# Kernel tuning notes

Hardware: AMD Instinct MI355X
Metric: run time of the kernel (lower is better)

The kernel has to match this reference:

```python
import jax, jax.numpy as jnp
import numpy as np

N = 50000      # nodes
E = 800000     # edges (avg degree 16)
IN, EMB, HID, OUT = 128, 256, 256, 128
KS = (25000, 12500)  # absolute top-k node counts per pooling level
NEG = -1e9


def setup_inputs() -> dict:
    key = jax.random.key(0)
    k = jax.random.split(key, 20)
    s = 0.05
    rn = lambda kk, shp: (jax.random.normal(kk, shp, jnp.float32) * s)
    return {
        "features": jax.random.normal(k[0], (N, IN), jnp.float32),
        "src": jax.random.randint(k[1], (E,), 0, N, dtype=jnp.int32),
        "dst": jax.random.randint(k[2], (E,), 0, N, dtype=jnp.int32),
        "W_embed": rn(k[3], (IN, EMB)), "b_embed": jnp.zeros((EMB,), jnp.float32),
        "W_enc0": rn(k[4], (EMB, HID)), "b_enc0": jnp.zeros((HID,), jnp.float32),
        "W_enc1": rn(k[5], (HID, HID)), "b_enc1": jnp.zeros((HID,), jnp.float32),
        "W_p0": rn(k[6], (HID, 1)), "b_p0": jnp.zeros((1,), jnp.float32),
        "W_p1": rn(k[7], (HID, 1)), "b_p1": jnp.zeros((1,), jnp.float32),
        "W_bot": rn(k[8], (HID, HID)), "b_bot": jnp.zeros((HID,), jnp.float32),
        "W_dec0": rn(k[9], (HID, HID)), "b_dec0": jnp.zeros((HID,), jnp.float32),
        "W_dec1": rn(k[10], (HID, OUT)), "b_dec1": jnp.zeros((OUT,), jnp.float32),
    }


def _gcn(h, src, dst, emask, W, b, act):
    """DGL GraphConv, norm='both': D_out^{-1/2} A D_in^{-1/2} h W + b, deg clamped >=1.
    emask: float [E] validity mask for edges of the current (sub)graph."""
    n = h.shape[0]
    deg_out = jnp.clip(jax.ops.segment_sum(emask, src, num_segments=n), 1.0)
    deg_in = jnp.clip(jax.ops.segment_sum(emask, dst, num_segments=n), 1.0)
    msg = (h * (deg_out ** -0.5)[:, None])[src] * emask[:, None]  # [E, F]
    agg = jax.ops.segment_sum(msg, dst, num_segments=n)
    out = (agg * (deg_in ** -0.5)[:, None]) @ W + b
    return jax.nn.relu(out) if act else out


def _forward(features, src, dst, W_embed, b_embed, W_enc0, b_enc0, W_enc1, b_enc1,
             W_p0, b_p0, W_p1, b_p1, W_bot, b_bot, W_dec0, b_dec0, W_dec1, b_dec1):
    n = features.shape[0]
    ones_e = jnp.ones((src.shape[0],), features.dtype)
    enc = [(W_enc0, b_enc0), (W_enc1, b_enc1)]
    pools = [(W_p0, b_p0), (W_p1, b_p1)]
    dec = [(W_dec0, b_dec0), (W_dec1, b_dec1)]
    L = len(KS)

    h = _gcn(features, src, dst, ones_e, W_embed, b_embed, True)
    masks = [jnp.ones((n,), features.dtype)]  # node mask per graph level
    hidden = []
    for i in range(L):  # encoder (dropout = eval-mode identity)
        m = masks[i]
        em = m[src] * m[dst]
        h = _gcn(h, src, dst, em, enc[i][0], enc[i][1], True) * m[:, None]
        hidden.append(h)
        # gPool: sigmoid projection score, top-k node selection, gate by score
        scores = jax.nn.sigmoid(h @ pools[i][0] + pools[i][1])[:, 0]
        _, idx = jax.lax.top_k(jnp.where(m > 0, scores, NEG), KS[i])
        nm = jnp.zeros((n,), features.dtype).at[idx].set(1.0)
        h = h * (scores * nm)[:, None]
        masks.append(nm)
    mL = masks[L]
    emL = mL[src] * mL[dst]
    h = _gcn(h, src, dst, emL, W_bot, b_bot, True) * mL[:, None]
    for i in range(L):  # decoder: gUnpool (identity under full-rep masking) + skip + GCN
        j = L - 1 - i
        h = h + hidden[j]
        m = masks[j]
        em = m[src] * m[dst]
        act = i < L - 1  # last decoder layer has no activation
        h = _gcn(h, src, dst, em, dec[i][0], dec[i][1], act) * m[:, None]
    return h


def reference(features, src, dst, W_embed, b_embed, W_enc0, b_enc0, W_enc1, b_enc1,
              W_p0, b_p0, W_p1, b_p1, W_bot, b_bot, W_dec0, b_dec0, W_dec1, b_dec1):
    return _forward(features, src, dst, W_embed, b_embed, W_enc0, b_enc0, W_enc1, b_enc1,
                    W_p0, b_p0, W_p1, b_p1, W_bot, b_bot, W_dec0, b_dec0, W_dec1, b_dec1)
```

## Files before the change

### kernel.cpp

```cpp
#include <hip/hip_runtime.h>
#include <hip/hip_bf16.h>
#include <type_traits>

__global__ void hist_kernel(const int* __restrict__ src, const int* __restrict__ dst,
                            int* __restrict__ deg_out, int* __restrict__ deg_in, int E) {
    int e = blockIdx.x * blockDim.x + threadIdx.x;
    if (e < E) {
        atomicAdd(&deg_out[src[e]], 1);
        atomicAdd(&deg_in[dst[e]], 1);
    }
}

__global__ void scan_kernel(const int* __restrict__ deg, int* __restrict__ row_ptr,
                            int* __restrict__ cursor, int n) {
    __shared__ int wsum[16];
    __shared__ int running;
    int tid = threadIdx.x, lane = tid & 63, wid = tid >> 6;
    if (tid == 0) running = 0;
    __syncthreads();
    for (int base = 0; base < n; base += 1024) {
        int i = base + tid;
        int v = (i < n) ? deg[i] : 0;
        int incl = v;
        #pragma unroll
// ... 158 lines not shown
    float tv = t[node];
    if (MASKED && tv == 0.f) return;
    int e0 = row_ptr[node], e1 = row_ptr[node + 1];
    const float4* X4 = (const float4*)X;
    float ax = 0.f, ay = 0.f, az = 0.f, aw = 0.f;
    int e = e0;
    for (; e + 3 < e1; e += 4) {
        int u0 = col[e], u1 = col[e + 1], u2 = col[e + 2], u3 = col[e + 3];
        float s0 = s[u0], s1 = s[u1], s2 = s[u2], s3 = s[u3];
        if (!MASKED) {
            float4 x0 = X4[(size_t)u0 * 64 + f4];
            float4 x1 = X4[(size_t)u1 * 64 + f4];
            float4 x2 = X4[(size_t)u2 * 64 + f4];
            float4 x3 = X4[(size_t)u3 * 64 + f4];
            ax += s0 * x0.x; ay += s0 * x0.y; az += s0 * x0.z; aw += s0 * x0.w;
            ax += s1 * x1.x; ay += s1 * x1.y; az += s1 * x1.z; aw += s1 * x1.w;
            ax += s2 * x2.x; ay += s2 * x2.y; az += s2 * x2.z; aw += s2 * x2.w;
            ax += s3 * x3.x; ay += s3 * x3.y; az += s3 * x3.z; aw += s3 * x3.w;
        } else {
            if (s0 != 0.f) { float4 x = X4[(size_t)u0 * 64 + f4];
                ax += s0 * x.x; ay += s0 * x.y; az += s0 * x.z; aw += s0 * x.w; }
            if (s1 != 0.f) { float4 x = X4[(size_t)u1 * 64 + f4];
                ax += s1 * x.x; ay += s1 * x.y; az += s1 * x.z; aw += s1 * x.w; }
            if (s2 != 0.f) { float4 x = X4[(size_t)u2 * 64 + f4];
                ax += s2 * x.x; ay += s2 * x.y; az += s2 * x.z; aw += s2 * x.w; }
            if (s3 != 0.f) { float4 x = X4[(size_t)u3 * 64 + f4];
                ax += s3 * x.x; ay += s3 * x.y; az += s3 * x.z; aw += s3 * x.w; }
        }
    }
    for (; e < e1; ++e) {
        int u = col[e];
        float sc = s[u];
        if (!MASKED || sc != 0.f) {
            float4 xv = X4[(size_t)u * 64 + f4];
            ax += sc * xv.x; ay += sc * xv.y; az += sc * xv.z; aw += sc * xv.w;
        }
    }
    if (SPLIT) {
        ushort4 hv, lv;
        split4(ax * tv, ay * tv, az * tv, aw * tv, hv, lv);
        *(ushort4*)&oh[(size_t)node * 256 + f4 * 4] = hv;
        *(ushort4*)&ol[(size_t)node * 256 + f4 * 4] = lv;
    } else {
        float4 r; r.x = ax * tv; r.y = ay * tv; r.z = az * tv; r.w = aw * tv;
        ((float4*)out)[(size_t)node * 64 + f4] = r;
    }
}

__global__ void agg_bias_128_kernel(const int* __restrict__ row_ptr, const int* __restrict__ col,
                                    const float* __restrict__ P, const float* __restrict__ t,
                                    const float* __restrict__ bias, float* __restrict__ out, int n) {
    int tid = threadIdx.x;
    int node = blockIdx.x * 8 + (tid >> 5);
    int f4 = tid & 31;
    if (node >= n) return;
    int e0 = row_ptr[node], e1 = row_ptr[node + 1];
    const float4* P4 = (const float4*)P;
    float ax = 0.f, ay = 0.f, az = 0.f, aw = 0.f;
    int e = e0;
    for (; e + 3 < e1; e += 4) {
        int u0 = col[e], u1 = col[e + 1], u2 = col[e + 2], u3 = col[e + 3];
        float4 x0 = P4[(size_t)u0 * 32 + f4];
        float4 x1 = P4[(size_t)u1 * 32 + f4];
        float4 x2 = P4[(size_t)u2 * 32 + f4];
        float4 x3 = P4[(size_t)u3 * 32 + f4];
        ax += x0.x; ay += x0.y; az += x0.z; aw += x0.w;
        ax += x1.x; ay += x1.y; az += x1.z; aw += x1.w;
        ax += x2.x; ay += x2.y; az += x2.z; aw += x2.w;
        ax += x3.x; ay += x3.y; az += x3.z; aw += x3.w;
    }
    for (; e < e1; ++e) {
        int u = col[e];
        float4 q = P4[(size_t)u * 32 + f4];
        ax += q.x; ay += q.y; az += q.z; aw += q.w;
    }
    float tv = t[node];
    float4 bv = ((const float4*)bias)[f4];
    float4 r;
    r.x = ax * tv + bv.x; r.y = ay * tv + bv.y;
    r.z = az * tv + bv.z; r.w = aw * tv + bv.w;
    ((float4*)out)[(size_t)node * 32 + f4] = r;
}

__global__ void add_split_kernel(const float* __restrict__ A, const float* __restrict__ B,
                                 const float* __restrict__ mask, const float* __restrict__ rs,
                                 unsigned short* __restrict__ oh, unsigned short* __restrict__ ol,
                                 int n4) {
    int i = blockIdx.x * blockDim.x + threadIdx.x;
    if (i >= n4) return;
    int row = i >> 6;
    float4 a = ((const float4*)A)[i];
    float4 b = ((const float4*)B)[i];
    if (mask[row] == 0.f) { a.x = 0.f; a.y = 0.f; a.z = 0.f; a.w = 0.f; }
    float r = rs[row];
    ushort4 hv, lv;
    split4((a.x + b.x) * r, (a.y + b.y) * r, (a.z + b.z) * r, (a.w + b.w) * r, hv, lv);
    size_t o = (size_t)row * 256 + (size_t)(i & 63) * 4;
    *(ushort4*)&oh[o] = hv;
    *(ushort4*)&ol[o] = lv;
}


__global__ void wsplit_all_kernel(const float* __restrict__ W0, const float* __restrict__ W1,
                                  const float* __restrict__ W2, const float* __restrict__ W3,
                                  const float* __restrict__ W4, const float* __restrict__ W5,
                                  unsigned short* __restrict__ H, unsigned short* __restrict__ L) {
    int i = blockIdx.x * blockDim.x + threadIdx.x;
    const float* W; int rel, base, outIdx;
    if (i < 32768) { W = W0; rel = i; base = 0;
        int k = rel >> 8, nn = rel & 255; outIdx = nn * 128 + k; }
    else if (i < 98304) { W = W1; rel = i - 32768; base = 32768;
        int k = rel >> 8, nn = rel & 255; outIdx = nn * 256 + k; }
    else if (i < 163840) { W = W2; rel = i - 98304; base = 98304;
        int k = rel >> 8, nn = rel & 255; outIdx = nn * 256 + k; }
    else if (i < 229376) { W = W3; rel = i - 163840; base = 163840;
        int k = rel >> 8, nn = rel & 255; outIdx = nn * 256 + k; }
    else if (i < 294912) { W = W4; rel = i - 229376; base = 229376;
        int k = rel >> 8, nn = rel & 255; outIdx = nn * 256 + k; }
    else { W = W5; rel = i - 294912; base = 294912;
        int k = rel >> 7, nn = rel & 127; outIdx = nn * 256 + k; }
    float x = W[rel];
    unsigned short h = f2bf(x);
    H[base + outIdx] = h;
    L[base + outIdx] = f2bf(x - bf2f(h));
}

template <bool RELU>
__global__ __launch_bounds__(256) void gemm_mfma_kernel(
    const unsigned short* __restrict__ Ah, const unsigned short* __restrict__ Al,
    const unsigned short* __restrict__ Wh, const unsigned short* __restrict__ Wl,
    const float* __restrict__ bias, float* __restrict__ C, int M, int K, int Nn) {
    __shared__ __align__(16) short sAh[64][40];
    __shared__ __align__(16) short sAl[64][40];
    __shared__ __align__(16) short sWh[128][40];
    __shared__ __align__(16) short sWl[128][40];
    int tid = threadIdx.x;
    int bm = blockIdx.x * 64, bn = blockIdx.y * 128;
    int lane = tid & 63, wid = tid >> 6;
    int lr = lane & 15, kg = lane >> 4;
    int arow = tid >> 2, akq = (tid & 3) * 8;
    int wn = tid >> 1, wkh = (tid & 1) * 16;
    const unsigned short* ahp = Ah + (size_t)(bm + arow) * K + akq;
    const unsigned short* alp = Al + (size_t)(bm + arow) * K + akq;
    const unsigned short* whp = Wh + (size_t)(bn + wn) * K + wkh;
    const unsigned short* wlp = Wl + (size_t)(bn + wn) * K + wkh;
    f32x4 acc[4][2];
    #pragma unroll
    for (int i = 0; i < 4; ++i)
        #pragma unroll
        for (int j = 0; j < 2; ++j) acc[i][j] = (f32x4){0.f, 0.f, 0.f, 0.f};
    for (int k0 = 0; k0 < K; k0 += 32) {
        short8v aH = *(const short8v*)(ahp + k0);
        short8v aL = *(const short8v*)(alp + k0);
        short8v w0 = *(const short8v*)(whp + k0);
        short8v w1 = *(const short8v*)(whp + k0 + 8);
        short8v w2 = *(const short8v*)(wlp + k0);
        short8v w3 = *(const short8v*)(wlp + k0 + 8);
        __syncthreads();
        *(short8v*)&sAh[arow][akq] = aH;
        *(short8v*)&sAl[arow][akq] = aL;
        *(short8v*)&sWh[wn][wkh] = w0;
        *(short8v*)&sWh[wn][wkh + 8] = w1;
        *(short8v*)&sWl[wn][wkh] = w2;
        *(short8v*)&sWl[wn][wkh + 8] = w3;
        __syncthreads();
        short8v ah[4], al[4], bh[2], bl[2];
        #pragma unroll
        for (int mf = 0; mf < 4; ++mf) {
            ah[mf] = *(const short8v*)&sAh[mf * 16 + lr][kg * 8];
            al[mf] = *(const short8v*)&sAl[mf * 16 + lr][kg * 8];
        }
        #pragma unroll
        for (int nf = 0; nf < 2; ++nf) {
            int c = wid * 32 + nf * 16 + lr;
            bh[nf] = *(const short8v*)&sWh[c][kg * 8];
            bl[nf] = *(const short8v*)&sWl[c][kg * 8];
        }
        #pragma unroll
        for (int mf = 0; mf < 4; ++mf)
            #pragma unroll
            for (int nf = 0; nf < 2; ++nf) {
                acc[mf][nf] = __builtin_amdgcn_mfma_f32_16x16x32_bf16(ah[mf], bh[nf], acc[mf][nf], 0, 0, 0);
                acc[mf][nf] = __builtin_amdgcn_mfma_f32_16x16x32_bf16(ah[mf], bl[nf], acc[mf][nf], 0, 0, 0);
                acc[mf][nf] = __builtin_amdgcn_mfma_f32_16x16x32_bf16(al[mf], bh[nf], acc[mf][nf], 0, 0, 0);
            }
    }
    #pragma unroll
    for (int mf = 0; mf < 4; ++mf) {
        #pragma unroll
        for (int nf = 0; nf < 2; ++nf) {
            int col = bn + wid * 32 + nf * 16 + lr;
            float bv = bias ? bias[col] : 0.f;
            #pragma unroll
            for (int r = 0; r < 4; ++r) {
                int grow = bm + mf * 16 + kg * 4 + r;
                if (grow < M) {
                    float x = acc[mf][nf][r] + bv;
                    if (RELU) x = fmaxf(x, 0.f);
                    C[(size_t)grow * Nn + col] = x;
                }
            }
        }
    }
}

template <bool RELU>
__global__ __launch_bounds__(256) void gemm_rows_mfma_kernel(
    const unsigned short* __restrict__ Ah, const unsigned short* __restrict__ Al,
    const unsigned short* __restrict__ Wh, const unsigned short* __restrict__ Wl,
    const float* __restrict__ bias, const int* __restrict__ idx, int Mc,
    float* __restrict__ C, int K, int Nn) {
    __shared__ __align__(16) short sAh[64][40];
    __shared__ __align__(16) short sAl[64][40];
    __shared__ __align__(16) short sWh[128][40];
    __shared__ __align__(16) short sWl[128][40];
    __shared__ int ridx[64];
    int tid = threadIdx.x;
    int bm = blockIdx.x * 64, bn = blockIdx.y * 128;
    int lane = tid & 63, wid = tid >> 6;
    int lr = lane & 15, kg = lane >> 4;
    int arow = tid >> 2, akq = (tid & 3) * 8;
    int wn = tid >> 1, wkh = (tid & 1) * 16;
    if (tid < 64) {
        int r = bm + tid;
        ridx[tid] = (r < Mc) ? idx[r] : idx[0];
    }
    __syncthreads();
    int rA = ridx[arow];
    const unsigned short* ahp = Ah + (size_t)rA * K + akq;
    const unsigned short* alp = Al + (size_t)rA * K + akq;
    const unsigned short* whp = Wh + (size_t)(bn + wn) * K + wkh;
    const unsigned short* wlp = Wl + (size_t)(bn + wn) * K + wkh;
    f32x4 acc[4][2];
    #pragma unroll
    for (int i = 0; i < 4; ++i)
        #pragma unroll
        for (int j = 0; j < 2; ++j) acc[i][j] = (f32x4){0.f, 0.f, 0.f, 0.f};
    for (int k0 = 0; k0 < K; k0 += 32) {
        short8v aH = *(const short8v*)(ahp + k0);
        short8v aL = *(const short8v*)(alp + k0);
        short8v w0 = *(const short8v*)(whp + k0);
        short8v w1 = *(const short8v*)(whp + k0 + 8);
        short8v w2 = *(const short8v*)(wlp + k0);
        short8v w3 = *(const short8v*)(wlp + k0 + 8);
        __syncthreads();
        *(short8v*)&sAh[arow][akq] = aH;
        *(short8v*)&sAl[arow][akq] = aL;
        *(short8v*)&sWh[wn][wkh] = w0;
        *(short8v*)&sWh[wn][wkh + 8] = w1;
        *(short8v*)&sWl[wn][wkh] = w2;
        *(short8v*)&sWl[wn][wkh + 8] = w3;
        __syncthreads();
        short8v ah[4], al[4], bh[2], bl[2];
        #pragma unroll
        for (int mf = 0; mf < 4; ++mf) {
            ah[mf] = *(const short8v*)&sAh[mf * 16 + lr][kg * 8];
            al[mf] = *(const short8v*)&sAl[mf * 16 + lr][kg * 8];
        }
        #pragma unroll
        for (int nf = 0; nf < 2; ++nf) {
            int c = wid * 32 + nf * 16 + lr;
            bh[nf] = *(const short8v*)&sWh[c][kg * 8];
            bl[nf] = *(const short8v*)&sWl[c][kg * 8];
        }
        #pragma unroll
        for (int mf = 0; mf < 4; ++mf)
            #pragma unroll
            for (int nf = 0; nf < 2; ++nf) {
                acc[mf][nf] = __builtin_amdgcn_mfma_f32_16x16x32_bf16(ah[mf], bh[nf], acc[mf][nf], 0, 0, 0);
                acc[mf][nf] = __builtin_amdgcn_mfma_f32_16x16x32_bf16(ah[mf], bl[nf], acc[mf][nf], 0, 0, 0);
                acc[mf][nf] = __builtin_amdgcn_mfma_f32_16x16x32_bf16(al[mf], bh[nf], acc[mf][nf], 0, 0, 0);
            }
    }
    #pragma unroll
    for (int mf = 0; mf < 4; ++mf) {
        #pragma unroll
        for (int nf = 0; nf < 2; ++nf) {
            int col = bn + wid * 32 + nf * 16 + lr;
            float bv = bias[col];
            #pragma unroll
            for (int r = 0; r < 4; ++r) {
                int lrow = mf * 16 + kg * 4 + r;
                if (bm + lrow < Mc) {
                    int grow = ridx[lrow];
                    float x = acc[mf][nf][r] + bv;
                    if (RELU) x = fmaxf(x, 0.f);
                    C[(size_t)grow * Nn + col] = x;
                }
            }
        }
    }
}

template <bool RELU>
__global__ __launch_bounds__(256) void gemm_kernel(const float* __restrict__ A,
                                                   const float* __restrict__ W,
                                                   const float* __restrict__ bias,
                                                   const float* __restrict__ mask,
                                                   const float* __restrict__ rowscale,
                                                   float* __restrict__ C, int M, int K, int Nn) {
    __shared__ float As[16][68];
    __shared__ float Bs[16][132];
    int tid = threadIdx.x;
    int bm = blockIdx.x * 64, bn = blockIdx.y * 128;
    int mA = tid >> 2, kqA = (tid & 3) * 4;
    int kB = tid >> 4, nqB = (tid & 15) * 8;
    int tm = (tid >> 4) * 4, tn = (tid & 15) * 4;
    float acc[4][8] = {};
    float rs = rowscale ? rowscale[bm + mA] : 1.f;
    for (int k0 = 0; k0 < K; k0 += 16) {
        float4 av = *(const float4*)(A + (size_t)(bm + mA) * K + k0 + kqA);
        As[kqA + 0][mA] = av.x * rs; As[kqA + 1][mA] = av.y * rs;
        As[kqA + 2][mA] = av.z * rs; As[kqA + 3][mA] = av.w * rs;
        const float* wp = W + (size_t)(k0 + kB) * Nn + bn + nqB;
        *(float4*)&Bs[kB][nqB]     = *(const float4*)wp;
        *(float4*)&Bs[kB][nqB + 4] = *(const float4*)(wp + 4);
        __syncthreads();
        #pragma unroll
        for (int kk = 0; kk < 16; ++kk) {
            float4 a  = *(const float4*)&As[kk][tm];
            float4 b0 = *(const float4*)&Bs[kk][tn];
            float4 b1 = *(const float4*)&Bs[kk][tn + 64];
            float ar[4] = {a.x, a.y, a.z, a.w};
            float br[8] = {b0.x, b0.y, b0.z, b0.w, b1.x, b1.y, b1.z, b1.w};
            #pragma unroll
            for (int i2 = 0; i2 < 4; i2++)
                #pragma unroll
                for (int j = 0; j < 8; j++) acc[i2][j] += ar[i2] * br[j];
        }
        __syncthreads();
    }
    #pragma unroll
    for (int i2 = 0; i2 < 4; i2++) {
        int row = bm + tm + i2;
        if (row < M) {
            float mv = mask ? mask[row] : 1.f;
            float o[8];
            #pragma unroll
            for (int j = 0; j < 8; j++) {
                int cj = (j < 4) ? (tn + j) : (64 + tn + j - 4);
                float x = acc[i2][j] + (bias ? bias[bn + cj] : 0.f);
                if (RELU) x = fmaxf(x, 0.f);
                o[j] = x * mv;
            }
            float* cp = C + (size_t)row * Nn + bn;
            *(float4*)(cp + tn)      = make_float4(o[0], o[1], o[2], o[3]);
            *(float4*)(cp + 64 + tn) = make_float4(o[4], o[5], o[6], o[7]);
        }
    }
}

__global__ void score_kernel(const float* __restrict__ H, const float* __restrict__ Wp,
                             const float* __restrict__ bp, const float* __restrict__ mask,
                             float* __restrict__ scores, float* __restrict__ keys, int n) {
    int lane = threadIdx.x & 63;
    int node = blockIdx.x * 4 + (threadIdx.x >> 6);
    if (node >= n) return;
    float4 hv = ((const float4*)(H + (size_t)node * 256))[lane];
    float4 wq = ((const float4*)Wp)[lane];
    float d = hv.x * wq.x + hv.y * wq.y + hv.z * wq.z + hv.w * wq.w;
    #pragma unroll
    for (int off = 32; off > 0; off >>= 1) d += __shfl_down(d, off);
    if (lane == 0) {
        float sc = 1.f / (1.f + expf(-(d + bp[0])));
        scores[node] = sc;
        keys[node] = (mask && mask[node] == 0.f) ? -1e9f : sc;
    }
}

__device__ __forceinline__ unsigned key_u(float f) {
    unsigned u = __float_as_uint(f);
// ... 127 lines not shown
    if (tid == 0) *tie_cnt = 0;
    int K = sel[1];
    int base = tid * 64;
    int local = 0;
    #pragma unroll 8
    for (int b = 0; b < 64; ++b) local += hist[base + b];
    arr[tid] = local;
    __syncthreads();
    for (int off = 1; off < 1024; off <<= 1) {
        int v = (tid + off < 1024) ? arr[tid + off] : 0;
        __syncthreads();
        arr[tid] += v;
        __syncthreads();
    }
    int above = arr[tid] - local;
    if (above < K && arr[tid] >= K) {
        int run = above;
        for (int b = base + 63; b >= base; --b) {
            int c = hist[b];
            if (run + c >= K) {
                sel[2] = (int)((((unsigned)sel[0]) << 16) | (unsigned)b);
                sel[3] = K - run;
                break;
            }
            run += c;
        }
    }
}

__global__ void topk_mark(const float* __restrict__ keys, const float* __restrict__ scores,
                          const int* __restrict__ sel, float* __restrict__ nm,
                          float* __restrict__ gate, int* __restrict__ tie_list,
                          int* __restrict__ tie_cnt, int n) {
    int i = blockIdx.x * blockDim.x + threadIdx.x;
    if (i >= n) return;
    unsigned Tkey = (unsigned)sel[2];
    unsigned u = key_u(keys[i]);
    float v = 0.f;
    if (u > Tkey) v = 1.f;
    else if (u == Tkey) { int p = atomicAdd(tie_cnt, 1); tie_list[p] = i; }
    nm[i] = v;
    gate[i] = v * scores[i];
}

__global__ void topk_ties(const float* __restrict__ scores, const int* __restrict__ sel,
                          const int* __restrict__ tie_list, const int* __restrict__ tie_cnt,
                          float* __restrict__ nm, float* __restrict__ gate) {
    int cnt = *tie_cnt;
    int need = sel[3];
    for (int j = threadIdx.x; j < cnt; j += blockDim.x) {
        int idx = tie_list[j];
        int rank = 0;
        for (int k2 = 0; k2 < cnt; ++k2) rank += (tie_list[k2] < idx) ? 1 : 0;
        if (rank < need) { nm[idx] = 1.f; gate[idx] = scores[idx]; }
    }
}

__global__ void compact_kernel(const float* __restrict__ nm, int* __restrict__ idx,
                               int* __restrict__ cnt, int n) {
    int i = blockIdx.x * blockDim.x + threadIdx.x;
    if (i < n && nm[i] != 0.f) {
        int p = atomicAdd(cnt, 1);
        idx[p] = i;
    }
}

__global__ void add_mask_kernel(float* __restrict__ A, const float* __restrict__ B,
                                const float* __restrict__ mask, int n4) {
    int i = blockIdx.x * blockDim.x + threadIdx.x;
    if (i < n4) {
        float4 a = ((float4*)A)[i];
        float4 b = ((const float4*)B)[i];
        if (mask && mask[i >> 6] == 0.f) { a.x = 0.f; a.y = 0.f; a.z = 0.f; a.w = 0.f; }
        a.x += b.x; a.y += b.y; a.z += b.z; a.w += b.w;
        ((float4*)A)[i] = a;
    }
}

extern "C" void kernel_launch(void* const* d_in, const int* in_sizes, int n_in,
                              void* d_out, int out_size, void* d_ws, size_t ws_size,
                              hipStream_t stream) {
    const int n = in_sizes[0] / 128;
    const int E = in_sizes[1];
    const int NPAD = ((n + 63) / 64) * 64;
    const int K1 = 25000, K2 = 12500;

    const float* features = (const float*)d_in[0];
    const int* src = (const int*)d_in[1];
    const int* dst = (const int*)d_in[2];
    const float* W_embed = (const float*)d_in[3];
    const float* b_embed = (const float*)d_in[4];
    const float* W_enc0  = (const float*)d_in[5];
    const float* b_enc0  = (const float*)d_in[6];
    const float* W_enc1  = (const float*)d_in[7];
    const float* b_enc1  = (const float*)d_in[8];
    const float* W_p0    = (const float*)d_in[9];
    const float* b_p0    = (const float*)d_in[10];
    const float* W_p1    = (const float*)d_in[11];
    const float* b_p1    = (const float*)d_in[12];
    const float* W_bot   = (const float*)d_in[13];
    const float* b_bot   = (const float*)d_in[14];
    const float* W_dec0  = (const float*)d_in[15];
    const float* b_dec0  = (const float*)d_in[16];
    const float* W_dec1  = (const float*)d_in[17];
    const float* b_dec1  = (const float*)d_in[18];
    float* out_f = (float*)d_out;

    char* ws = (char*)d_ws;
    size_t off = 0;
    auto alloc = [&](size_t bytes) -> void* {
        void* p = ws + off;
        off += (bytes + 255) & ~(size_t)255;
        return p;
    };
    (void)alloc(256);
    int* row_ptr  = (int*)alloc((size_t)(n + 1) * 4);
    int* cursor   = (int*)alloc((size_t)n * 4);
    int* col      = (int*)alloc((size_t)E * 4);
    int* deg_out_i= (int*)alloc((size_t)n * 4);
    int* deg_in_i = (int*)alloc((size_t)n * 4);
    float* so_m1  = (float*)alloc((size_t)n * 4);
    float* si_m1  = (float*)alloc((size_t)n * 4);
    float* so_m2  = (float*)alloc((size_t)n * 4);
    float* si_m2  = (float*)alloc((size_t)n * 4);
    float* sarr   = (float*)alloc((size_t)n * 4);
    float* tarr   = (float*)alloc((size_t)n * 4);
    float* scores1= (float*)alloc((size_t)n * 4);
    float* keys1  = (float*)alloc((size_t)n * 4);
    float* scores2= (float*)alloc((size_t)n * 4);
    float* keys2  = (float*)alloc((size_t)n * 4);
    float* nm1    = (float*)alloc((size_t)n * 4);
    float* gate1  = (float*)alloc((size_t)n * 4);
    float* nm2    = (float*)alloc((size_t)n * 4);
    float* gate2  = (float*)alloc((size_t)n * 4);
    size_t big = (size_t)NPAD * 256 * 4;
    float* A = (float*)alloc(big);
    float* B = (float*)alloc(big);
    float* C = (float*)alloc(big);
    float* D = (float*)alloc(big);
    unsigned short* Dh = (unsigned short*)D;
    unsigned short* Dl = Dh + (size_t)NPAD * 256;
    unsigned short* Dh128 = Dh;
    unsigned short* Dl128 = Dh + (size_t)NPAD * 128;
    int* rhist    = (int*)alloc(65536 * 4);
    int* sel      = (int*)alloc(256);
    int* tie_cnt  = (int*)alloc(256);
    int* tie_list = (int*)alloc((size_t)n * 4);
    float* s0     = (float*)alloc((size_t)n * 4);
    float* t0     = (float*)alloc((size_t)n * 4);
    int* idx1     = (int*)alloc((size_t)n * 4);
    int* idx2     = (int*)alloc((size_t)n * 4);
    int* ccnt     = (int*)alloc(256);
    const int WO_EMBED = 0, WO_ENC0 = 32768, WO_ENC1 = 98304,
              WO_BOT = 163840, WO_DEC0 = 229376, WO_DEC1 = 294912;
    const int WTOT = 327680;
    unsigned short* wsph = (unsigned short*)alloc((size_t)WTOT * 2);
    unsigned short* wspl = (unsigned short*)alloc((size_t)WTOT * 2);
    bool fast = (off <= ws_size);

    dim3 blk(256);
    int gE = (E + 255) / 256;
    int gN = (n + 255) / 256;
    int gAgg256 = (n + 3) / 4;
    int gAgg128 = (n + 7) / 8;
    int gScore = (n + 3) / 4;
    dim3 gemm_g(NPAD / 64, 2);
    dim3 gemm_g128(NPAD / 64, 1);
    dim3 gemm_gK1((K1 + 63) / 64, 2);
    dim3 gemm_gK2((K2 + 63) / 64, 2);
    int gAdd = (n * 64 + 255) / 256;

    auto run_topk = [&](const float* keys, const float* scores, float* nm, float* gate, int K) {
        if (fast) {
            hipMemsetAsync(rhist, 0, 65536 * 4, stream);
            topk_hist1<<<gN, blk, 0, stream>>>(keys, n, rhist);
            topk_scan1<<<1, 1024, 0, stream>>>(rhist, K, sel);
            hipMemsetAsync(rhist, 0, 65536 * 4, stream);
            topk_hist2<<<gN, blk, 0, stream>>>(keys, n, sel, rhist);
            topk_scan2<<<1, 1024, 0, stream>>>(rhist, sel, tie_cnt);
            topk_mark<<<gN, blk, 0, stream>>>(keys, scores, sel, nm, gate, tie_list, tie_cnt, n);
            topk_ties<<<1, 256, 0, stream>>>(scores, sel, tie_list, tie_cnt, nm, gate);
        } else {
            topk_kernel<<<1, 1024, 0, stream>>>(keys, scores, nm, gate, n, K);
        }
    };
    float* sF = fast ? s0 : sarr;
    float* tF = fast ? t0 : tarr;

    if (fast) {
        wsplit_all_kernel<<<WTOT / 256, blk, 0, stream>>>(W_embed, W_enc0, W_enc1, W_bot,
                                                          W_dec0, W_dec1, wsph, wspl);
    }

    hipMemsetAsync(deg_out_i, 0, (size_t)n * 4, stream);
    hipMemsetAsync(deg_in_i, 0, (size_t)n * 4, stream);
    hist_kernel<<<gE, blk, 0, stream>>>(src, dst, deg_out_i, deg_in_i, E);
    scan_kernel<<<1, 1024, 0, stream>>>(deg_in_i, row_ptr, cursor, n);
    fill_kernel<<<gE, blk, 0, stream>>>(src, dst, cursor, col, E);
    sort_rows_kernel<<<gN, blk, 0, stream>>>(row_ptr, col, n);

    scale_full_kernel<<<gN, blk, 0, stream>>>(deg_out_i, deg_in_i, sF, tF, n);

    if (fast) {
        agg_feat_128_kernel<true><<<gAgg128, blk, 0, stream>>>(row_ptr, col, features, sF, tF,
                                                               nullptr, Dh128, Dl128, n);
        gemm_mfma_kernel<true><<<gemm_g, blk, 0, stream>>>(Dh128, Dl128, wsph + WO_EMBED,
                                                           wspl + WO_EMBED, b_embed, A, n, 128, 256);
    } else {
        agg_feat_128_kernel<false><<<gAgg128, blk, 0, stream>>>(row_ptr, col, features, sF, tF,
                                                                D, nullptr, nullptr, n);
        gemm_kernel<true><<<gemm_g, blk, 0, stream>>>(D, W_embed, b_embed, nullptr, nullptr, A, n, 128, 256);
    }

    if (fast) {
        agg_f32_256_kernel<false, true><<<gAgg256, blk, 0, stream>>>(row_ptr, col, A, sF, tF,
                                                                     nullptr, Dh, Dl, n);
        gemm_mfma_kernel<true><<<gemm_g, blk, 0, stream>>>(Dh, Dl, wsph + WO_ENC0, wspl + WO_ENC0,
                                                           b_enc0, B, n, 256, 256);
    } else {
        agg_f32_256_kernel<false, false><<<gAgg256, blk, 0, stream>>>(row_ptr, col, A, sF, tF,
                                                                      D, nullptr, nullptr, n);
        gemm_kernel<true><<<gemm_g, blk, 0, stream>>>(D, W_enc0, b_enc0, nullptr, nullptr, B, n, 256, 256);
    }

    score_kernel<<<gScore, blk, 0, stream>>>(B, W_p0, b_p0, nullptr, scores1, keys1, n);
    run_topk(keys1, scores1, nm1, gate1, K1);
    if (fast) {
        hipMemsetAsync(ccnt, 0, 4, stream);
        compact_kernel<<<gN, blk, 0, stream>>>(nm1, idx1, ccnt, n);
    }

    hipMemsetAsync(so_m1, 0, (size_t)n * 4, stream);
    out_deg_mask_kernel<<<gE, blk, 0, stream>>>(src, dst, nm1, so_m1, E);
    in_deg_mask_kernel<<<gN, blk, 0, stream>>>(row_ptr, col, nm1, si_m1, n);
    scale_mask_kernel<<<gN, blk, 0, stream>>>(gate1, nm1, so_m1, si_m1, sarr, tarr, n);
    if (fast) {
        agg_f32_256_kernel<true, true><<<gAgg256, blk, 0, stream>>>(row_ptr, col, B, sarr, tarr,
                                                                    nullptr, Dh, Dl, n);
        gemm_rows_mfma_kernel<true><<<gemm_gK1, blk, 0, stream>>>(Dh, Dl, wsph + WO_ENC1,
                                                                  wspl + WO_ENC1, b_enc1, idx1, K1, C, 256, 256);
    } else {
        agg_f32_256_kernel<true, false><<<gAgg256, blk, 0, stream>>>(row_ptr, col, B, sarr, tarr,
                                                                     D, nullptr, nullptr, n);
        gemm_kernel<true><<<gemm_g, blk, 0, stream>>>(D, W_enc1, b_enc1, nm1, nullptr, C, n, 256, 256);
    }

    score_kernel<<<gScore, blk, 0, stream>>>(C, W_p1, b_p1, nm1, scores2, keys2, n);
    run_topk(keys2, scores2, nm2, gate2, K2);
    if (fast) {
        hipMemsetAsync(ccnt + 1, 0, 4, stream);
        compact_kernel<<<gN, blk, 0, stream>>>(nm2, idx2, ccnt + 1, n);
    }

    hipMemsetAsync(so_m2, 0, (size_t)n * 4, stream);
    out_deg_mask_kernel<<<gE, blk, 0, stream>>>(src, dst, nm2, so_m2, E);
    in_deg_mask_kernel<<<gN, blk, 0, stream>>>(row_ptr, col, nm2, si_m2, n);
    scale_mask_kernel<<<gN, blk, 0, stream>>>(gate2, nm2, so_m2, si_m2, sarr, tarr, n);
    if (fast) {
        agg_f32_256_kernel<true, true><<<gAgg256, blk, 0, stream>>>(row_ptr, col, C, sarr, tarr,
                                                                    nullptr, Dh, Dl, n);
        gemm_rows_mfma_kernel<true><<<gemm_gK2, blk, 0, stream>>>(Dh, Dl, wsph + WO_BOT,
                                                                  wspl + WO_BOT, b_bot, idx2, K2, A, 256, 256);
    } else {
        agg_f32_256_kernel<true, false><<<gAgg256, blk, 0, stream>>>(row_ptr, col, C, sarr, tarr,
                                                                     D, nullptr, nullptr, n);
        gemm_kernel<true><<<gemm_g, blk, 0, stream>>>(D, W_bot, b_bot, nm2, nullptr, A, n, 256, 256);
    }

    add_mask_kernel<<<gAdd, blk, 0, stream>>>(A, C, fast ? nm2 : nullptr, n * 64);
    scale_mask_kernel<<<gN, blk, 0, stream>>>(nm1, nm1, so_m1, si_m1, sarr, tarr, n);
    if (fast) {
        agg_f32_256_kernel<true, true><<<gAgg256, blk, 0, stream>>>(row_ptr, col, A, sarr, tarr,
                                                                    nullptr, Dh, Dl, n);
        gemm_rows_mfma_kernel<true><<<gemm_gK1, blk, 0, stream>>>(Dh, Dl, wsph + WO_DEC0,
                                                                  wspl + WO_DEC0, b_dec0, idx1, K1, A, 256, 256);
    } else {
        agg_f32_256_kernel<true, false><<<gAgg256, blk, 0, stream>>>(row_ptr, col, A, sarr, tarr,
                                                                     D, nullptr, nullptr, n);
        gemm_kernel<true><<<gemm_g, blk, 0, stream>>>(D, W_dec0, b_dec0, nm1, nullptr, A, n, 256, 256);
    }

    if (fast) {
        add_split_kernel<<<gAdd, blk, 0, stream>>>(A, B, nm1, sF, Dh, Dl, n * 64);
        gemm_mfma_kernel<false><<<gemm_g128, blk, 0, stream>>>(Dh, Dl, wsph + WO_DEC1,
                                                               wspl + WO_DEC1, nullptr, C, n, 256, 128);
    } else {
        add_mask_kernel<<<gAdd, blk, 0, stream>>>(A, B, nullptr, n * 64);
        scale_full_kernel<<<gN, blk, 0, stream>>>(deg_out_i, deg_in_i, sarr, tarr, n);
        gemm_kernel<false><<<gemm_g128, blk, 0, stream>>>(A, W_dec1, nullptr, nullptr, sF, C, n, 256, 128);
    }
    agg_bias_128_kernel<<<gAgg128, blk, 0, stream>>>(row_ptr, col, C, tF, b_dec1, out_f, n);

    (void)n_in; (void)out_size;
}
```

Before: 1.146 ms.

## Enlarge MFMA GEMM tiles to 128x128 and fuse add-split into dec1 GEMM

The split-bf16 MFMA GEMM kernels move from a 64x128 tile to a 128x128 tile, with each wave computing a 64x64 sub-tile. This gives more reuse per LDS load and halves the number of row blocks. The last decoder layer's add, mask, scale and bf16 hi/lo split is fused into the GEMM A-tile load, so the intermediate Dh/Dl buffers are no longer written and re-read. The two degree memsets are merged into one. The cost is more LDS and registers per block, which may lower occupancy, and the padded row count changes, so grids for the fallback path use separate dimensions.

Result: no change. 1.143 ms (-0.3%).

```diff
diff --git a/kernel.cpp b/kernel.cpp
--- a/kernel.cpp
+++ b/kernel.cpp
@@ -264,24 +264,6 @@
     ((float4*)out)[(size_t)node * 32 + f4] = r;
 }
 
-__global__ void add_split_kernel(const float* __restrict__ A, const float* __restrict__ B,
-                                 const float* __restrict__ mask, const float* __restrict__ rs,
-                                 unsigned short* __restrict__ oh, unsigned short* __restrict__ ol,
-                                 int n4) {
-    int i = blockIdx.x * blockDim.x + threadIdx.x;
-    if (i >= n4) return;
-    int row = i >> 6;
-    float4 a = ((const float4*)A)[i];
-    float4 b = ((const float4*)B)[i];
-    if (mask[row] == 0.f) { a.x = 0.f; a.y = 0.f; a.z = 0.f; a.w = 0.f; }
-    float r = rs[row];
-    ushort4 hv, lv;
-    split4((a.x + b.x) * r, (a.y + b.y) * r, (a.z + b.z) * r, (a.w + b.w) * r, hv, lv);
-    size_t o = (size_t)row * 256 + (size_t)(i & 63) * 4;
-    *(ushort4*)&oh[o] = hv;
-    *(ushort4*)&ol[o] = lv;
-}
-
 
 __global__ void wsplit_all_kernel(const float* __restrict__ W0, const float* __restrict__ W1,
                                   const float* __restrict__ W2, const float* __restrict__ W3,
@@ -308,74 +290,71 @@
 }
 
 template <bool RELU>
-__global__ __launch_bounds__(256) void gemm_mfma_kernel(
+__global__ __launch_bounds__(256, 3) void gemm_mfma_kernel(
     const unsigned short* __restrict__ Ah, const unsigned short* __restrict__ Al,
     const unsigned short* __restrict__ Wh, const unsigned short* __restrict__ Wl,
     const float* __restrict__ bias, float* __restrict__ C, int M, int K, int Nn) {
-    __shared__ __align__(16) short sAh[64][40];
-    __shared__ __align__(16) short sAl[64][40];
+    __shared__ __align__(16) short sAh[128][40];
+    __shared__ __align__(16) short sAl[128][40];
     __shared__ __align__(16) short sWh[128][40];
     __shared__ __align__(16) short sWl[128][40];
     int tid = threadIdx.x;
-    int bm = blockIdx.x * 64, bn = blockIdx.y * 128;
+    int bm = blockIdx.x * 128, bn = blockIdx.y * 128;
     int lane = tid & 63, wid = tid >> 6;
+    int wr = (wid >> 1) * 64, wc = (wid & 1) * 64;
     int lr = lane & 15, kg = lane >> 4;
-    int arow = tid >> 2, akq = (tid & 3) * 8;
-    int wn = tid >> 1, wkh = (tid & 1) * 16;
+    int arow = tid >> 1, akq = (tid & 1) * 16;
     const unsigned short* ahp = Ah + (size_t)(bm + arow) * K + akq;
     const unsigned short* alp = Al + (size_t)(bm + arow) * K + akq;
-    const unsigned short* whp = Wh + (size_t)(bn + wn) * K + wkh;
-    const unsigned short* wlp = Wl + (size_t)(bn + wn) * K + wkh;
-    f32x4 acc[4][2];
+    const unsigned short* whp = Wh + (size_t)(bn + arow) * K + akq;
+    const unsigned short* wlp = Wl + (size_t)(bn + arow) * K + akq;
+    f32x4 acc[4][4];
     #pragma unroll
     for (int i = 0; i < 4; ++i)
         #pragma unroll
-        for (int j = 0; j < 2; ++j) acc[i][j] = (f32x4){0.f, 0.f, 0.f, 0.f};
+        for (int j = 0; j < 4; ++j) acc[i][j] = (f32x4){0.f, 0.f, 0.f, 0.f};
     for (int k0 = 0; k0 < K; k0 += 32) {
-        short8v aH = *(const short8v*)(ahp + k0);
-        short8v aL = *(const short8v*)(alp + k0);
+        short8v a0 = *(const short8v*)(ahp + k0);
+        short8v a1 = *(const short8v*)(ahp + k0 + 8);
+        short8v l0 = *(const short8v*)(alp + k0);
+        short8v l1 = *(const short8v*)(alp + k0 + 8);
         short8v w0 = *(const short8v*)(whp + k0);
         short8v w1 = *(const short8v*)(whp + k0 + 8);
-        short8v w2 = *(const short8v*)(wlp + k0);
-        short8v w3 = *(const short8v*)(wlp + k0 + 8);
-        __syncthreads();
-        *(short8v*)&sAh[arow][akq] = aH;
-        *(short8v*)&sAl[arow][akq] = aL;
-        *(short8v*)&sWh[wn][wkh] = w0;
-        *(short8v*)&sWh[wn][wkh + 8] = w1;
-        *(short8v*)&sWl[wn][wkh] = w2;
-        *(short8v*)&sWl[wn][wkh + 8] = w3;
-        __syncthreads();
-        short8v ah[4], al[4], bh[2], bl[2];
+        short8v v0 = *(const short8v*)(wlp + k0);
+        short8v v1 = *(const short8v*)(wlp + k0 + 8);
+        __syncthreads();
+        *(short8v*)&sAh[arow][akq] = a0; *(short8v*)&sAh[arow][akq + 8] = a1;
+        *(short8v*)&sAl[arow][akq] = l0; *(short8v*)&sAl[arow][akq + 8] = l1;
+        *(short8v*)&sWh[arow][akq] = w0; *(short8v*)&sWh[arow][akq + 8] = w1;
+        *(short8v*)&sWl[arow][akq] = v0; *(short8v*)&sWl[arow][akq + 8] = v1;
+        __syncthreads();
+        short8v ah[4], al[4];
         #pragma unroll
         for (int mf = 0; mf < 4; ++mf) {
-            ah[mf] = *(const short8v*)&sAh[mf * 16 + lr][kg * 8];
-            al[mf] = *(const short8v*)&sAl[mf * 16 + lr][kg * 8];
-        }
-        #pragma unroll
-        for (int nf = 0; nf < 2; ++nf) {
-            int c = wid * 32 + nf * 16 + lr;
-            bh[nf] = *(const short8v*)&sWh[c][kg * 8];
-            bl[nf] = *(const short8v*)&sWl[c][kg * 8];
-        }
-        #pragma unroll
-        for (int mf = 0; mf < 4; ++mf)
+            ah[mf] = *(const short8v*)&sAh[wr + mf * 16 + lr][kg * 8];
+            al[mf] = *(const short8v*)&sAl[wr + mf * 16 + lr][kg * 8];
+        }
+        #pragma unroll
+        for (int nf = 0; nf < 4; ++nf) {
+            short8v bh = *(const short8v*)&sWh[wc + nf * 16 + lr][kg * 8];
+            short8v bl = *(const short8v*)&sWl[wc + nf * 16 + lr][kg * 8];
             #pragma unroll
-            for (int nf = 0; nf < 2; ++nf) {
-                acc[mf][nf] = __builtin_amdgcn_mfma_f32_16x16x32_bf16(ah[mf], bh[nf], acc[mf][nf], 0, 0, 0);
-                acc[mf][nf] = __builtin_amdgcn_mfma_f32_16x16x32_bf16(ah[mf], bl[nf], acc[mf][nf], 0, 0, 0);
-                acc[mf][nf] = __builtin_amdgcn_mfma_f32_16x16x32_bf16(al[mf], bh[nf], acc[mf][nf], 0, 0, 0);
+            for (int mf = 0; mf < 4; ++mf) {
+                acc[mf][nf] = __builtin_amdgcn_mfma_f32_16x16x32_bf16(ah[mf], bh, acc[mf][nf], 0, 0, 0);
+                acc[mf][nf] = __builtin_amdgcn_mfma_f32_16x16x32_bf16(ah[mf], bl, acc[mf][nf], 0, 0, 0);
+                acc[mf][nf] = __builtin_amdgcn_mfma_f32_16x16x32_bf16(al[mf], bh, acc[mf][nf], 0, 0, 0);
             }
+        }
     }
     #pragma unroll
     for (int mf = 0; mf < 4; ++mf) {
         #pragma unroll
-        for (int nf = 0; nf < 2; ++nf) {
-            int col = bn + wid * 32 + nf * 16 + lr;
+        for (int nf = 0; nf < 4; ++nf) {
+            int col = bn + wc + nf * 16 + lr;
             float bv = bias ? bias[col] : 0.f;
             #pragma unroll
             for (int r = 0; r < 4; ++r) {
-                int grow = bm + mf * 16 + kg * 4 + r;
+                int grow = bm + wr + mf * 16 + kg * 4 + r;
                 if (grow < M) {
                     float x = acc[mf][nf][r] + bv;
                     if (RELU) x = fmaxf(x, 0.f);
@@ -387,23 +366,23 @@
 }
 
 template <bool RELU>
-__global__ __launch_bounds__(256) void gemm_rows_mfma_kernel(
+__global__ __launch_bounds__(256, 3) void gemm_rows_mfma_kernel(
     const unsigned short* __restrict__ Ah, const unsigned short* __restrict__ Al,
     const unsigned short* __restrict__ Wh, const unsigned short* __restrict__ Wl,
     const float* __restrict__ bias, const int* __restrict__ idx, int Mc,
     float* __restrict__ C, int K, int Nn) {
-    __shared__ __align__(16) short sAh[64][40];
-    __shared__ __align__(16) short sAl[64][40];
+    __shared__ __align__(16) short sAh[128][40];
+    __shared__ __align__(16) short sAl[128][40];
     __shared__ __align__(16) short sWh[128][40];
     __shared__ __align__(16) short sWl[128][40];
-    __shared__ int ridx[64];
+    __shared__ int ridx[128];
     int tid = threadIdx.x;
-    int bm = blockIdx.x * 64, bn = blockIdx.y * 128;
+    int bm = blockIdx.x * 128, bn = blockIdx.y * 128;
     int lane = tid & 63, wid = tid >> 6;
+    int wr = (wid >> 1) * 64, wc = (wid & 1) * 64;
     int lr = lane & 15, kg = lane >> 4;
-    int arow = tid >> 2, akq = (tid & 3) * 8;
-    int wn = tid >> 1, wkh = (tid & 1) * 16;
-    if (tid < 64) {
+    int arow = tid >> 1, akq = (tid & 1) * 16;
+    if (tid < 128) {
         int r = bm + tid;
         ridx[tid] = (r < Mc) ? idx[r] : idx[0];
     }
@@ -411,64 +390,146 @@
     int rA = ridx[arow];
     const unsigned short* ahp = Ah + (size_t)rA * K + akq;
     const unsigned short* alp = Al + (size_t)rA * K + akq;
-    const unsigned short* whp = Wh + (size_t)(bn + wn) * K + wkh;
-    const unsigned short* wlp = Wl + (size_t)(bn + wn) * K + wkh;
-    f32x4 acc[4][2];
+    const unsigned short* whp = Wh + (size_t)(bn + arow) * K + akq;
+    const unsigned short* wlp = Wl + (size_t)(bn + arow) * K + akq;
+    f32x4 acc[4][4];
     #pragma unroll
     for (int i = 0; i < 4; ++i)
         #pragma unroll
-        for (int j = 0; j < 2; ++j) acc[i][j] = (f32x4){0.f, 0.f, 0.f, 0.f};
+        for (int j = 0; j < 4; ++j) acc[i][j] = (f32x4){0.f, 0.f, 0.f, 0.f};
     for (int k0 = 0; k0 < K; k0 += 32) {
-        short8v aH = *(const short8v*)(ahp + k0);
-        short8v aL = *(const short8v*)(alp + k0);
+        short8v a0 = *(const short8v*)(ahp + k0);
+        short8v a1 = *(const short8v*)(ahp + k0 + 8);
+        short8v l0 = *(const short8v*)(alp + k0);
+        short8v l1 = *(const short8v*)(alp + k0 + 8);
         short8v w0 = *(const short8v*)(whp + k0);
         short8v w1 = *(const short8v*)(whp + k0 + 8);
-        short8v w2 = *(const short8v*)(wlp + k0);
-        short8v w3 = *(const short8v*)(wlp + k0 + 8);
-        __syncthreads();
-        *(short8v*)&sAh[arow][akq] = aH;
-        *(short8v*)&sAl[arow][akq] = aL;
-        *(short8v*)&sWh[wn][wkh] = w0;
-        *(short8v*)&sWh[wn][wkh + 8] = w1;
-        *(short8v*)&sWl[wn][wkh] = w2;
-        *(short8v*)&sWl[wn][wkh + 8] = w3;
-        __syncthreads();
-        short8v ah[4], al[4], bh[2], bl[2];
+        short8v v0 = *(const short8v*)(wlp + k0);
+        short8v v1 = *(const short8v*)(wlp + k0 + 8);
+        __syncthreads();
+        *(short8v*)&sAh[arow][akq] = a0; *(short8v*)&sAh[arow][akq + 8] = a1;
+        *(short8v*)&sAl[arow][akq] = l0; *(short8v*)&sAl[arow][akq + 8] = l1;
+        *(short8v*)&sWh[arow][akq] = w0; *(short8v*)&sWh[arow][akq + 8] = w1;
+        *(short8v*)&sWl[arow][akq] = v0; *(short8v*)&sWl[arow][akq + 8] = v1;
+        __syncthreads();
+        short8v ah[4], al[4];
         #pragma unroll
         for (int mf = 0; mf < 4; ++mf) {
-            ah[mf] = *(const short8v*)&sAh[mf * 16 + lr][kg * 8];
-            al[mf] = *(const short8v*)&sAl[mf * 16 + lr][kg * 8];
-        }
-        #pragma unroll
-        for (int nf = 0; nf < 2; ++nf) {
-            int c = wid * 32 + nf * 16 + lr;
-            bh[nf] = *(const short8v*)&sWh[c][kg * 8];
-            bl[nf] = *(const short8v*)&sWl[c][kg * 8];
-        }
-        #pragma unroll
-        for (int mf = 0; mf < 4; ++mf)
+            ah[mf] = *(const short8v*)&sAh[wr + mf * 16 + lr][kg * 8];
+            al[mf] = *(const short8v*)&sAl[wr + mf * 16 + lr][kg * 8];
+        }
+        #pragma unroll
+        for (int nf = 0; nf < 4; ++nf) {
+            short8v bh = *(const short8v*)&sWh[wc + nf * 16 + lr][kg * 8];
+            short8v bl = *(const short8v*)&sWl[wc + nf * 16 + lr][kg * 8];
             #pragma unroll
-            for (int nf = 0; nf < 2; ++nf) {
-                acc[mf][nf] = __builtin_amdgcn_mfma_f32_16x16x32_bf16(ah[mf], bh[nf], acc[mf][nf], 0, 0, 0);
-                acc[mf][nf] = __builtin_amdgcn_mfma_f32_16x16x32_bf16(ah[mf], bl[nf], acc[mf][nf], 0, 0, 0);
-                acc[mf][nf] = __builtin_amdgcn_mfma_f32_16x16x32_bf16(al[mf], bh[nf], acc[mf][nf], 0, 0, 0);
+            for (int mf = 0; mf < 4; ++mf) {
+                acc[mf][nf] = __builtin_amdgcn_mfma_f32_16x16x32_bf16(ah[mf], bh, acc[mf][nf], 0, 0, 0);
+                acc[mf][nf] = __builtin_amdgcn_mfma_f32_16x16x32_bf16(ah[mf], bl, acc[mf][nf], 0, 0, 0);
+                acc[mf][nf] = __builtin_amdgcn_mfma_f32_16x16x32_bf16(al[mf], bh, acc[mf][nf], 0, 0, 0);
             }
+        }
     }
     #pragma unroll
     for (int mf = 0; mf < 4; ++mf) {
         #pragma unroll
-        for (int nf = 0; nf < 2; ++nf) {
-            int col = bn + wid * 32 + nf * 16 + lr;
+        for (int nf = 0; nf < 4; ++nf) {
+            int col = bn + wc + nf * 16 + lr;
             float bv = bias[col];
             #pragma unroll
             for (int r = 0; r < 4; ++r) {
-                int lrow = mf * 16 + kg * 4 + r;
+                int lrow = wr + mf * 16 + kg * 4 + r;
                 if (bm + lrow < Mc) {
                     int grow = ridx[lrow];
                     float x = acc[mf][nf][r] + bv;
                     if (RELU) x = fmaxf(x, 0.f);
                     C[(size_t)grow * Nn + col] = x;
                 }
+            }
+        }
+    }
+}
+
+__global__ __launch_bounds__(256, 3) void gemm_dec1_kernel(
+    const float* __restrict__ A, const float* __restrict__ B,
+    const float* __restrict__ mask, const float* __restrict__ rs,
+    const unsigned short* __restrict__ Wh, const unsigned short* __restrict__ Wl,
+    float* __restrict__ C, int M, int K) {
+    __shared__ __align__(16) short sAh[128][40];
+    __shared__ __align__(16) short sAl[128][40];
+    __shared__ __align__(16) short sWh[128][40];
+    __shared__ __align__(16) short sWl[128][40];
+    const int Nn = 128;
+    int tid = threadIdx.x;
+    int bm = blockIdx.x * 128, bn = 0;
+    int lane = tid & 63, wid = tid >> 6;
+    int wr = (wid >> 1) * 64, wc = (wid & 1) * 64;
+    int lr = lane & 15, kg = lane >> 4;
+    int arow = tid >> 1, akq = (tid & 1) * 16;
+    float mv = (mask[bm + arow] != 0.f) ? 1.f : 0.f;
+    float rsv = rs[bm + arow];
+    const float* apf = A + (size_t)(bm + arow) * K + akq;
+    const float* bpf = B + (size_t)(bm + arow) * K + akq;
+    const unsigned short* whp = Wh + (size_t)(bn + arow) * K + akq;
+    const unsigned short* wlp = Wl + (size_t)(bn + arow) * K + akq;
+    f32x4 acc[4][4];
+    #pragma unroll
+    for (int i = 0; i < 4; ++i)
+        #pragma unroll
+        for (int j = 0; j < 4; ++j) acc[i][j] = (f32x4){0.f, 0.f, 0.f, 0.f};
+    for (int k0 = 0; k0 < K; k0 += 32) {
+        const float4* pa = (const float4*)(apf + k0);
+        const float4* pb = (const float4*)(bpf + k0);
+        float4 qa0 = pa[0], qa1 = pa[1], qa2 = pa[2], qa3 = pa[3];
+        float4 qb0 = pb[0], qb1 = pb[1], qb2 = pb[2], qb3 = pb[3];
+        ushort4 h0, l0v, h1, l1v, h2, l2v, h3, l3v;
+        split4((qa0.x * mv + qb0.x) * rsv, (qa0.y * mv + qb0.y) * rsv,
+               (qa0.z * mv + qb0.z) * rsv, (qa0.w * mv + qb0.w) * rsv, h0, l0v);
+        split4((qa1.x * mv + qb1.x) * rsv, (qa1.y * mv + qb1.y) * rsv,
+               (qa1.z * mv + qb1.z) * rsv, (qa1.w * mv + qb1.w) * rsv, h1, l1v);
+        split4((qa2.x * mv + qb2.x) * rsv, (qa2.y * mv + qb2.y) * rsv,
+               (qa2.z * mv + qb2.z) * rsv, (qa2.w * mv + qb2.w) * rsv, h2, l2v);
+        split4((qa3.x * mv + qb3.x) * rsv, (qa3.y * mv + qb3.y) * rsv,
+               (qa3.z * mv + qb3.z) * rsv, (qa3.w * mv + qb3.w) * rsv, h3, l3v);
+        short8v w0 = *(const short8v*)(whp + k0);
+        short8v w1 = *(const short8v*)(whp + k0 + 8);
+        short8v v0 = *(const short8v*)(wlp + k0);
+        short8v v1 = *(const short8v*)(wlp + k0 + 8);
+        __syncthreads();
+        *(ushort4*)&sAh[arow][akq]      = h0; *(ushort4*)&sAh[arow][akq + 4]  = h1;
+        *(ushort4*)&sAh[arow][akq + 8]  = h2; *(ushort4*)&sAh[arow][akq + 12] = h3;
+        *(ushort4*)&sAl[arow][akq]      = l0v; *(ushort4*)&sAl[arow][akq + 4]  = l1v;
+        *(ushort4*)&sAl[arow][akq + 8]  = l2v; *(ushort4*)&sAl[arow][akq + 12] = l3v;
+        *(short8v*)&sWh[arow][akq] = w0; *(short8v*)&sWh[arow][akq + 8] = w1;
+        *(short8v*)&sWl[arow][akq] = v0; *(short8v*)&sWl[arow][akq + 8] = v1;
+        __syncthreads();
+        short8v ah[4], al[4];
+        #pragma unroll
+        for (int mf = 0; mf < 4; ++mf) {
+            ah[mf] = *(const short8v*)&sAh[wr + mf * 16 + lr][kg * 8];
+            al[mf] = *(const short8v*)&sAl[wr + mf * 16 + lr][kg * 8];
+        }
+        #pragma unroll
+        for (int nf = 0; nf < 4; ++nf) {
+            short8v bh = *(const short8v*)&sWh[wc + nf * 16 + lr][kg * 8];
+            short8v bl = *(const short8v*)&sWl[wc + nf * 16 + lr][kg * 8];
+            #pragma unroll
+            for (int mf = 0; mf < 4; ++mf) {
+                acc[mf][nf] = __builtin_amdgcn_mfma_f32_16x16x32_bf16(ah[mf], bh, acc[mf][nf], 0, 0, 0);
+                acc[mf][nf] = __builtin_amdgcn_mfma_f32_16x16x32_bf16(ah[mf], bl, acc[mf][nf], 0, 0, 0);
+                acc[mf][nf] = __builtin_amdgcn_mfma_f32_16x16x32_bf16(al[mf], bh, acc[mf][nf], 0, 0, 0);
+            }
+        }
+    }
+    #pragma unroll
+    for (int mf = 0; mf < 4; ++mf) {
+        #pragma unroll
+        for (int nf = 0; nf < 4; ++nf) {
+            int col = bn + wc + nf * 16 + lr;
+            #pragma unroll
+            for (int r = 0; r < 4; ++r) {
+                int grow = bm + wr + mf * 16 + kg * 4 + r;
+                if (grow < M) C[(size_t)grow * Nn + col] = acc[mf][nf][r];
             }
         }
     }
@@ -762,7 +823,7 @@
                               hipStream_t stream) {
     const int n = in_sizes[0] / 128;
     const int E = in_sizes[1];
-    const int NPAD = ((n + 63) / 64) * 64;
+    const int NPAD = ((n + 127) / 128) * 128;
     const int K1 = 25000, K2 = 12500;
 
     const float* features = (const float*)d_in[0];
@@ -844,10 +905,12 @@
     int gAgg256 = (n + 3) / 4;
     int gAgg128 = (n + 7) / 8;
     int gScore = (n + 3) / 4;
-    dim3 gemm_g(NPAD / 64, 2);
-    dim3 gemm_g128(NPAD / 64, 1);
-    dim3 gemm_gK1((K1 + 63) / 64, 2);
-    dim3 gemm_gK2((K2 + 63) / 64, 2);
+    dim3 gemm_g(NPAD / 128, 2);
+    dim3 gemm_g128(NPAD / 128, 1);
+    dim3 gemm_gK1((K1 + 127) / 128, 2);
+    dim3 gemm_gK2((K2 + 127) / 128, 2);
+    dim3 gemm_gv(NPAD / 64, 2);
+    dim3 gemm_gv128(NPAD / 64, 1);
     int gAdd = (n * 64 + 255) / 256;
 
     auto run_topk = [&](const float* keys, const float* scores, float* nm, float* gate, int K) {
@@ -872,8 +935,10 @@
                                                           W_dec0, W_dec1, wsph, wspl);
     }
 
-    hipMemsetAsync(deg_out_i, 0, (size_t)n * 4, stream);
-    hipMemsetAsync(deg_in_i, 0, (size_t)n * 4, stream);
+    {
+        size_t degpad = (((size_t)n * 4) + 255) & ~(size_t)255;
+        hipMemsetAsync(deg_out_i, 0, degpad + (size_t)n * 4, stream);
+    }
     hist_kernel<<<gE, blk, 0, stream>>>(src, dst, deg_out_i, deg_in_i, E);
     scan_kernel<<<1, 1024, 0, stream>>>(deg_in_i, row_ptr, cursor, n);
     fill_kernel<<<gE, blk, 0, stream>>>(src, dst, cursor, col, E);
@@ -889,7 +954,7 @@
     } else {
         agg_feat_128_kernel<false><<<gAgg128, blk, 0, stream>>>(row_ptr, col, features, sF, tF,
                                                                 D, nullptr, nullptr, n);
-        gemm_kernel<true><<<gemm_g, blk, 0, stream>>>(D, W_embed, b_embed, nullptr, nullptr, A, n, 128, 256);
+        gemm_kernel<true><<<gemm_gv, blk, 0, stream>>>(D, W_embed, b_embed, nullptr, nullptr, A, n, 128, 256);
     }
 
     if (fast) {
@@ -900,7 +965,7 @@
     } else {
         agg_f32_256_kernel<false, false><<<gAgg256, blk, 0, stream>>>(row_ptr, col, A, sF, tF,
                                                                       D, nullptr, nullptr, n);
-        gemm_kernel<true><<<gemm_g, blk, 0, stream>>>(D, W_enc0, b_enc0, nullptr, nullptr, B, n, 256, 256);
+        gemm_kernel<true><<<gemm_gv, blk, 0, stream>>>(D, W_enc0, b_enc0, nullptr, nullptr, B, n, 256, 256);
     }
 
     score_kernel<<<gScore, blk, 0, stream>>>(B, W_p0, b_p0, nullptr, scores1, keys1, n);
@@ -922,7 +987,7 @@
     } else {
         agg_f32_256_kernel<true, false><<<gAgg256, blk, 0, stream>>>(row_ptr, col, B, sarr, tarr,
                                                                      D, nullptr, nullptr, n);
-        gemm_kernel<true><<<gemm_g, blk, 0, stream>>>(D, W_enc1, b_enc1, nm1, nullptr, C, n, 256, 256);
+        gemm_kernel<true><<<gemm_gv, blk, 0, stream>>>(D, W_enc1, b_enc1, nm1, nullptr, C, n, 256, 256);
     }
 
     score_kernel<<<gScore, blk, 0, stream>>>(C, W_p1, b_p1, nm1, scores2, keys2, n);
@@ -944,7 +1009,7 @@
     } else {
         agg_f32_256_kernel<true, false><<<gAgg256, blk, 0, stream>>>(row_ptr, col, C, sarr, tarr,
                                                                      D, nullptr, nullptr, n);
-        gemm_kernel<true><<<gemm_g, blk, 0, stream>>>(D, W_bot, b_bot, nm2, nullptr, A, n, 256, 256);
+        gemm_kernel<true><<<gemm_gv, blk, 0, stream>>>(D, W_bot, b_bot, nm2, nullptr, A, n, 256, 256);
     }
 
     add_mask_kernel<<<gAdd, blk, 0, stream>>>(A, C, fast ? nm2 : nullptr, n * 64);
@@ -957,17 +1022,16 @@
     } else {
         agg_f32_256_kernel<true, false><<<gAgg256, blk, 0, stream>>>(row_ptr, col, A, sarr, tarr,
                                                                      D, nullptr, nullptr, n);
-        gemm_kernel<true><<<gemm_g, blk, 0, stream>>>(D, W_dec0, b_dec0, nm1, nullptr, A, n, 256, 256);
+        gemm_kernel<true><<<gemm_gv, blk, 0, stream>>>(D, W_dec0, b_dec0, nm1, nullptr, A, n, 256, 256);
     }
 
     if (fast) {
-        add_split_kernel<<<gAdd, blk, 0, stream>>>(A, B, nm1, sF, Dh, Dl, n * 64);
-        gemm_mfma_kernel<false><<<gemm_g128, blk, 0, stream>>>(Dh, Dl, wsph + WO_DEC1,
-                                                               wspl + WO_DEC1, nullptr, C, n, 256, 128);
+        gemm_dec1_kernel<<<gemm_g128, blk, 0, stream>>>(A, B, nm1, sF, wsph + WO_DEC1,
+                                                        wspl + WO_DEC1, C, n, 256);
     } else {
         add_mask_kernel<<<gAdd, blk, 0, stream>>>(A, B, nullptr, n * 64);
         scale_full_kernel<<<gN, blk, 0, stream>>>(deg_out_i, deg_in_i, sarr, tarr, n);
-        gemm_kernel<false><<<gemm_g128, blk, 0, stream>>>(A, W_dec1, nullptr, nullptr, sF, C, n, 256, 128);
+        gemm_kernel<false><<<gemm_gv128, blk, 0, stream>>>(A, W_dec1, nullptr, nullptr, sF, C, n, 256, 128);
     }
     agg_bias_128_kernel<<<gAgg128, blk, 0, stream>>>(row_ptr, col, C, tF, b_dec1, out_f, n);
 
```
